# Optimization experiments

Measured on AMD Instinct MI355X. Metric: run time of the kernel, lower is better.

Reference implementation:

```python
import jax, jax.numpy as jnp
import numpy as np

N, E, H, RBF, NZ = 15000, 300000, 128, 20, 119
CUTOFF, BOX = 6.0, 7.0


def setup_inputs() -> dict:
    key = jax.random.key(0)
    ks = jax.random.split(key, 24)
    s = 0.05

    def rn(k, shape):
        return jax.random.normal(k, shape, dtype=jnp.float32) * s

    z = jax.random.randint(ks[0], (N,), 0, 83)
    pos = jax.random.uniform(ks[1], (N, 3), dtype=jnp.float32) * BOX
    src = jax.random.randint(ks[2], (E,), 0, N)
    dst = (src + jax.random.randint(ks[3], (E,), 1, N)) % N  # guarantees src != dst
    edge_index = jnp.stack([src, dst], axis=0)  # (2, E)
    cell_offsets = (jax.random.randint(ks[4], (E, 3), 0, 3) - 1).astype(jnp.float32)
    cell = jnp.eye(3, dtype=jnp.float32) * BOX
    return dict(
        z=z, pos=pos, edge_index=edge_index, cell_offsets=cell_offsets, cell=cell,
        embed=rn(ks[5], (NZ, H)),
        msg_w1=rn(ks[6], (3, H, H)), msg_b1=rn(ks[7], (3, H)),
        msg_w2=rn(ks[8], (3, H, 3 * H)), msg_b2=rn(ks[9], (3, 3 * H)),
        filt_w=rn(ks[10], (3, RBF, 3 * H)), filt_b=rn(ks[11], (3, 3 * H)),
        upd_uw=rn(ks[12], (3, H, H)), upd_ub=rn(ks[13], (3, H)),
        upd_vw=rn(ks[14], (3, H, H)), upd_vb=rn(ks[15], (3, H)),
        upd_mw1=rn(ks[16], (3, 2 * H, H)), upd_mb1=rn(ks[17], (3, H)),
        upd_mw2=rn(ks[18], (3, H, 3 * H)), upd_mb2=rn(ks[19], (3, 3 * H)),
        head_w1=rn(ks[20], (H, H)), head_b1=rn(ks[21], (H,)),
        head_w2=rn(ks[22], (H, H)), head_b2=rn(ks[23], (H,)),
    )


def reference(z, pos, edge_index, cell_offsets, cell, embed,
              msg_w1, msg_b1, msg_w2, msg_b2, filt_w, filt_b,
              upd_uw, upd_ub, upd_vw, upd_vb,
              upd_mw1, upd_mb1, upd_mw2, upd_mb2,
              head_w1, head_b1, head_w2, head_b2):
    n_nodes = z.shape[0]
    hdim = embed.shape[1]
    row, col = edge_index[0], edge_index[1]  # receiver, sender (DeepDFT convention)

    # get_pbc_distances
    offsets = cell_offsets @ cell                                  # (E,3)
    edge_diff = pos[row] - pos[col] + offsets                      # (E,3)
    edge_dist = jnp.linalg.norm(edge_diff, axis=-1)                # (E,)
    unit = edge_diff / edge_dist[:, None]                          # (E,3)

    # sinc radial basis + cosine cutoff (shared by all message layers)
    n = jnp.arange(1, RBF + 1, dtype=pos.dtype)
    rbf = jnp.sin(edge_dist[:, None] * n * jnp.pi / CUTOFF) / edge_dist[:, None]  # (E,RBF)
    fcut = jnp.where(edge_dist < CUTOFF,
                     0.5 * (jnp.cos(jnp.pi * edge_dist / CUTOFF) + 1.0), 0.0)      # (E,)

    ns = embed[z]                                                  # (N,H)
    nv = jnp.zeros((n_nodes, 3, hdim), dtype=pos.dtype)            # (N,3,H)

    for i in range(3):
        # ---- PainnMessage ----
        filt = (rbf @ filt_w[i] + filt_b[i]) * fcut[:, None]       # (E,3H)
        sout = jax.nn.silu(ns @ msg_w1[i] + msg_b1[i]) @ msg_w2[i] + msg_b2[i]  # (N,3H)
        fo = filt * sout[col]                                      # (E,3H)
        gate_v, gate_e, msg_s = jnp.split(fo, 3, axis=1)           # each (E,H)
        msg_v = nv[col] * gate_v[:, None, :] + gate_e[:, None, :] * unit[:, :, None]  # (E,3,H)
        ns = ns + jax.ops.segment_sum(msg_s, row, num_segments=n_nodes)
        nv = nv + jax.ops.segment_sum(msg_v, row, num_segments=n_nodes)
        # ---- PainnUpdate ----
        Uv = nv @ upd_uw[i] + upd_ub[i]                            # (N,3,H)
        Vv = nv @ upd_vw[i] + upd_vb[i]                            # (N,3,H)
        mlp_in = jnp.concatenate([jnp.linalg.norm(Vv, axis=1), ns], axis=1)  # (N,2H)
        m = jax.nn.silu(mlp_in @ upd_mw1[i] + upd_mb1[i]) @ upd_mw2[i] + upd_mb2[i]  # (N,3H)
        a_vv, a_sv, a_ss = jnp.split(m, 3, axis=1)
        inner = jnp.sum(Uv * Vv, axis=1)                           # (N,H)
        nv = nv + a_vv[:, None, :] * Uv
        ns = ns + a_sv * inner + a_ss

    v = jax.nn.silu(ns @ head_w1 + head_b1) @ head_w2 + head_b2    # (N,H)
    return v, edge_dist
```

## Files before the change

kernel.cpp:

```cpp
#include <hip/hip_runtime.h>
#include <math.h>

#define HD 128
#define H3 384
#define RBF_N 20
#define CUTOFF_R 6.0f
#define PI_F 3.14159265358979323846f
#define CAPE 40000

#define PITCH 136

typedef __attribute__((ext_vector_type(8))) short short8v;
typedef __attribute__((ext_vector_type(4))) short short4v;
typedef __attribute__((ext_vector_type(4))) float f32x4;
typedef unsigned short bf_t;

__device__ __forceinline__ float silu_f(float x) { return x / (1.0f + __expf(-x)); }

__device__ __forceinline__ ushort f2bf(float f) {
    union { float f; uint u; } v; v.f = f;
    return (ushort)((v.u + 0x7FFF + ((v.u >> 16) & 1)) >> 16);
}
__device__ __forceinline__ float bf2f(ushort x) {
    union { uint u; float f; } v; v.u = ((uint)x) << 16;
    return v.f;
}
__device__ __forceinline__ short4v f2bf4(float4 x) {
    short4v r;
    r[0] = (short)f2bf(x.x); r[1] = (short)f2bf(x.y);
    r[2] = (short)f2bf(x.z); r[3] = (short)f2bf(x.w);
    return r;
}
__device__ __forceinline__ float4 b2f4(short4v x) {
    return make_float4(bf2f((ushort)x[0]), bf2f((ushort)x[1]),
                       bf2f((ushort)x[2]), bf2f((ushort)x[3]));
}

#define LOADWG(r, CNT, NTH, W, rowlen, koff)                                   \
    _Pragma("unroll")                                                          \
    for (int it_ = 0; it_ < CNT; ++it_) {                                      \
        int u_ = tid + it_ * NTH;                                              \
        (r)[it_] = *(const short8v*)((W) + (size_t)(u_ >> 4) * (rowlen) +      \
                                     (koff) + ((u_ & 15) << 3));               \
    }
#define COMMITWG(r, CNT, NTH)                                                  \
    _Pragma("unroll")                                                          \
    for (int it_ = 0; it_ < CNT; ++it_) {                                      \
        int u_ = tid + it_ * NTH;                                              \
        *(short8v*)&Wt[(u_ >> 4) * PITCH + ((u_ & 15) << 3)] = (r)[it_];       \
    }
#define MFMA4R(Abuf, acc)                                                      \
    _Pragma("unroll")                                                          \
    for (int step_ = 0; step_ < 4; ++step_) {                                  \
        int kb_ = step_ * 32 + lk;                                             \
        short8v a_ = *(const short8v*)&(Abuf)[(wr + lr) * PITCH + kb_];        \
        (acc) = __builtin_amdgcn_mfma_f32_16x16x32_bf16(                       \
            a_, *(const short8v*)&Wt[(wn + lr) * PITCH + kb_], (acc), 0, 0, 0);\
    }
#define MFMA8R(Abuf, acc)                                                      \
    _Pragma("unroll")                                                          \
    for (int step_ = 0; step_ < 4; ++step_) {                                  \
        int kb_ = step_ * 32 + lk;                                             \
        short8v a_ = *(const short8v*)&(Abuf)[(wr + lr) * PITCH + kb_];        \
        (acc)[0] = __builtin_amdgcn_mfma_f32_16x16x32_bf16(                    \
            a_, *(const short8v*)&Wt[(wn + lr) * PITCH + kb_], (acc)[0], 0, 0, 0); \
        (acc)[1] = __builtin_amdgcn_mfma_f32_16x16x32_bf16(                    \
            a_, *(const short8v*)&Wt[(wn + 16 + lr) * PITCH + kb_], (acc)[1], 0, 0, 0); \
    }

__global__ void geom_kernel(const float* __restrict__ pos, const int* __restrict__ ei,
                            const float* __restrict__ cofs, const float* __restrict__ cell,
                            float* __restrict__ dist_out, int* __restrict__ deg, int E) {
    int e = blockIdx.x * blockDim.x + threadIdx.x;
    if (e >= E) return;
    int r = ei[e], c = ei[E + e];
    float c0 = cofs[3*e], c1 = cofs[3*e+1], c2 = cofs[3*e+2];
    float d0 = pos[3*r]   - pos[3*c]   + c0*cell[0] + c1*cell[3] + c2*cell[6];
    float d1 = pos[3*r+1] - pos[3*c+1] + c0*cell[1] + c1*cell[4] + c2*cell[7];
    float d2 = pos[3*r+2] - pos[3*c+2] + c0*cell[2] + c1*cell[5] + c2*cell[8];
    float dist = sqrtf(d0*d0 + d1*d1 + d2*d2);
    dist_out[e] = dist;
    if (dist < CUTOFF_R) atomicAdd(&deg[r], 1);
}

__global__ void scan_kernel(const int* __restrict__ deg, int* __restrict__ off,
                            int* __restrict__ cursor, int n) {
    __shared__ int wsum[16];
    __shared__ int carry_s;
    const int tid = threadIdx.x;
    const int lane = tid & 63, wv = tid >> 6;
    if (tid == 0) carry_s = 0;
    __syncthreads();
    for (int base = 0; base < n; base += 1024) {
        int v = (base + tid < n) ? deg[base + tid] : 0;
        int x = v;
        #pragma unroll
        for (int s = 1; s < 64; s <<= 1) {
            int y = __shfl_up(x, s);
            if (lane >= s) x += y;
        }
        if (lane == 63) wsum[wv] = x;
        __syncthreads();
        if (tid == 0) {
            int a = carry_s;
            #pragma unroll
            for (int i = 0; i < 16; ++i) { int t = wsum[i]; wsum[i] = a; a += t; }
            carry_s = a;
        }
        __syncthreads();
        int exc = wsum[wv] + x - v;
        if (base + tid < n) { off[base + tid] = exc; cursor[base + tid] = exc; }
        __syncthreads();
    }
    if (tid == 0) off[n] = carry_s;
}

__global__ void scatter_kernel(const float* __restrict__ pos, const int* __restrict__ ei,
                               const float* __restrict__ cofs, const float* __restrict__ cell,
                               const float* __restrict__ dist_in, int* __restrict__ cursor,
                               int* __restrict__ col_s, float* __restrict__ fcut_s,
                               float* __restrict__ unit_s, float* __restrict__ rbf_s, int E) {
    int e = blockIdx.x * blockDim.x + threadIdx.x;
    if (e >= E) return;
    float dist = dist_in[e];
    if (!(dist < CUTOFF_R)) return;
    int r = ei[e], c = ei[E + e];
    float c0 = cofs[3*e], c1 = cofs[3*e+1], c2 = cofs[3*e+2];
    float d0 = pos[3*r]   - pos[3*c]   + c0*cell[0] + c1*cell[3] + c2*cell[6];
    float d1 = pos[3*r+1] - pos[3*c+1] + c0*cell[1] + c1*cell[4] + c2*cell[7];
    float d2 = pos[3*r+2] - pos[3*c+2] + c0*cell[2] + c1*cell[5] + c2*cell[8];
    int p = atomicAdd(&cursor[r], 1);
    if (p >= CAPE) return;
    col_s[p] = c;
    fcut_s[p] = 0.5f * (cosf(PI_F * dist / CUTOFF_R) + 1.0f);
    float inv = 1.0f / dist;
    unit_s[3*p]   = d0 * inv;
    unit_s[3*p+1] = d1 * inv;
    unit_s[3*p+2] = d2 * inv;
    #pragma unroll
    for (int j = 0; j < RBF_N; ++j)
        rbf_s[(size_t)p*RBF_N + j] = sinf(dist * (float)(j+1) * (PI_F / CUTOFF_R)) * inv;
}

__device__ __forceinline__ void wcvt(const float* __restrict__ src, bf_t* __restrict__ dst,
                                     int idx, int K, int N) {
    int per = K * N;
    int l = idx / per, r = idx % per;
    int k = r / N, n = r % N;
    dst[(size_t)l*per + (size_t)n*K + k] = f2bf(src[(size_t)l*per + (size_t)k*N + n]);
}

__global__ void wprep_kernel(const float* s0, const float* s1, const float* s2, const float* s3,
                             const float* s4, const float* s5, const float* s6, const float* s7,
                             bf_t* __restrict__ dst) {
    int i = blockIdx.x * blockDim.x + threadIdx.x;
    if (i < 49152)        wcvt(s0, dst + 0,      i - 0,      128, 128);
    else if (i < 196608)  wcvt(s1, dst + 49152,  i - 49152,  128, 384);
    else if (i < 245760)  wcvt(s2, dst + 196608, i - 196608, 128, 128);
    else if (i < 294912)  wcvt(s3, dst + 245760, i - 245760, 128, 128);
    else if (i < 393216)  wcvt(s4, dst + 294912, i - 294912, 256, 128);
    else if (i < 540672)  wcvt(s5, dst + 393216, i - 393216, 128, 384);
    else if (i < 557056)  wcvt(s6, dst + 540672, i - 540672, 128, 128);
    else if (i < 573440)  wcvt(s7, dst + 557056, i - 557056, 128, 128);
}

__global__ __launch_bounds__(512) void msg_mlp0(const int* __restrict__ z,
                                                const float* __restrict__ emb,
                                                bf_t* __restrict__ nsb,
                                                const bf_t* __restrict__ W1b,
                                                const float* __restrict__ b1,
                                                const bf_t* __restrict__ W2b,
                                                const float* __restrict__ b2,
                                                bf_t* __restrict__ Cb, int M) {
    __shared__ ushort As[32 * PITCH];
    __shared__ ushort Wt[128 * PITCH];
    __shared__ ushort Hid[32 * PITCH];
    const int tid = threadIdx.x;
    const int m0 = blockIdx.x * 32;
    const int wid = tid >> 6, lane = tid & 63;
    const int wr = (wid >> 2) * 16;
    const int wn = (wid & 3) * 32;
    const int lr = lane & 15, lk = (lane >> 4) << 3;
    const int er = (lane >> 4) << 2;

    short8v rwA[4], rwB[4];
    LOADWG(rwA, 4, 512, W1b, 128, 0);
    {
        int row = tid >> 4, k8 = (tid & 15) << 3;
        int m = m0 + row;
        short8v pk = (short8v)(0);
        if (m < M) {
            const float* ep = emb + (size_t)z[m] * HD + k8;
            const float4 x = *(const float4*)ep, y = *(const float4*)(ep + 4);
            pk[0]=(short)f2bf(x.x); pk[1]=(short)f2bf(x.y);
            pk[2]=(short)f2bf(x.z); pk[3]=(short)f2bf(x.w);
            pk[4]=(short)f2bf(y.x); pk[5]=(short)f2bf(y.y);
            pk[6]=(short)f2bf(y.z); pk[7]=(short)f2bf(y.w);
            *(short8v*)(nsb + (size_t)m * HD + k8) = pk;
        }
        *(short8v*)&As[row * PITCH + k8] = pk;
    }
    __syncthreads();
    COMMITWG(rwA, 4, 512); LOADWG(rwB, 4, 512, W2b, 128, 0);
    __syncthreads();
    f32x4 acc1[2];
    acc1[0] = (f32x4)(0.f); acc1[1] = (f32x4)(0.f);
    MFMA8R(As, acc1);
    __syncthreads();
    COMMITWG(rwB, 4, 512); LOADWG(rwA, 4, 512, W2b + 16384, 128, 0);
    #pragma unroll
    for (int j = 0; j < 2; ++j) {
        int col = wn + 16 * j + lr;
        float bb = b1[col];
        #pragma unroll
        for (int r = 0; r < 4; ++r)
            Hid[(wr + er + r) * PITCH + col] = f2bf(silu_f(acc1[j][r] + bb));
    }
    __syncthreads();
    {
        f32x4 a0[2]; a0[0] = (f32x4)(0.f); a0[1] = (f32x4)(0.f);
        MFMA8R(Hid, a0);
        __syncthreads();
        COMMITWG(rwA, 4, 512); LOADWG(rwB, 4, 512, W2b + 32768, 128, 0);
        #pragma unroll
        for (int j = 0; j < 2; ++j) {
            int col = wn + 16 * j + lr;
            float bb = b2[col];
            #pragma unroll
            for (int r = 0; r < 4; ++r) {
                int m = m0 + wr + er + r;
                if (m < M) Cb[(size_t)m * H3 + col] = f2bf(a0[j][r] + bb);
            }
        }
        __syncthreads();
    }
    {
        f32x4 a1[2]; a1[0] = (f32x4)(0.f); a1[1] = (f32x4)(0.f);
        MFMA8R(Hid, a1);
        __syncthreads();
        COMMITWG(rwB, 4, 512);
        #pragma unroll
        for (int j = 0; j < 2; ++j) {
            int col = wn + 16 * j + lr;
            float bb = b2[128 + col];
            #pragma unroll
            for (int r = 0; r < 4; ++r) {
                int m = m0 + wr + er + r;
                if (m < M) Cb[(size_t)m * H3 + 128 + col] = f2bf(a1[j][r] + bb);
            }
        }
        __syncthreads();
    }
    {
        f32x4 a2[2]; a2[0] = (f32x4)(0.f); a2[1] = (f32x4)(0.f);
        MFMA8R(Hid, a2);
        #pragma unroll
        for (int j = 0; j < 2; ++j) {
            int col = wn + 16 * j + lr;
            float bb = b2[256 + col];
            #pragma unroll
            for (int r = 0; r < 4; ++r) {
                int m = m0 + wr + er + r;
                if (m < M) Cb[(size_t)m * H3 + 256 + col] = f2bf(a2[j][r] + bb);
            }
        }
    }
}

template <int MODE>
__global__ __launch_bounds__(1024) void upd_fused(const bf_t* __restrict__ nv2p,
                                                 const bf_t* __restrict__ Ub,
                                                 const bf_t* __restrict__ Vb,
                                                 const float* __restrict__ bu,
                                                 const float* __restrict__ bv,
                                                 bf_t* __restrict__ nvp,
                                                 bf_t* __restrict__ nsb,
                                                 const bf_t* __restrict__ W1b,
                                                 const float* __restrict__ b1,
                                                 const bf_t* __restrict__ W2b,
                                                 const float* __restrict__ b2,
                                                 const bf_t* __restrict__ xw1,
                                                 const float* __restrict__ xb1,
                                                 const bf_t* __restrict__ xw2,
                                                 const float* __restrict__ xb2,
                                                 bf_t* __restrict__ soutb,
                                                 float* __restrict__ Cf,
                                                 int N) {
    __shared__ ushort As3[3][32 * PITCH];
    __shared__ ushort Wt[128 * PITCH];
    __shared__ ushort nrmL[32 * PITCH];
    __shared__ ushort Hid[32 * PITCH];
    __shared__ ushort AsG[32 * PITCH];
    const int tid = threadIdx.x;
    const int m0 = blockIdx.x * 32;
    const int wid = tid >> 6, lane = tid & 63;
    const int wr = (wid >> 3) * 16;
    const int wn = (wid & 7) * 16;
    const int lr = lane & 15, lk = (lane >> 4) << 3;
    const int er = (lane >> 4) << 2;
    const size_t NHD = (size_t)N * HD;

    short8v rwA[2], rwB[2];
    LOADWG(rwA, 2, 1024, Ub, 128, 0);

    #pragma unroll
    for (int it = 0; it < 2; ++it) {
        int u = tid + it * 1024;
        if (u < 1536) {
            int d = u >> 9, v = u & 511;
            int row = v >> 4, k8 = (v & 15) << 3;
            int m = m0 + row;
            short8v pk = (short8v)(0);
            if (m < N) pk = *(const short8v*)(nv2p + (size_t)d * NHD + (size_t)m * HD + k8);
            *(short8v*)&As3[d][row * PITCH + k8] = pk;
        }
    }
    if (tid < 512) {
        int row = tid >> 4, k8 = (tid & 15) << 3;
        int m = m0 + row;
        short8v pk = (short8v)(0);
        if (m < N) pk = *(const short8v*)(nsb + (size_t)m * HD + k8);
        *(short8v*)&AsG[row * PITCH + k8] = pk;
    }
    __syncthreads();
    COMMITWG(rwA, 2, 1024); LOADWG(rwB, 2, 1024, Vb, 128, 0);
    __syncthreads();

    f32x4 aU[3], aV[3];
    #pragma unroll
    for (int d = 0; d < 3; ++d) { aU[d] = (f32x4)(0.f); aV[d] = (f32x4)(0.f); }
    #pragma unroll
    for (int d = 0; d < 3; ++d) { MFMA4R(As3[d], aU[d]); }
    __syncthreads();
    COMMITWG(rwB, 2, 1024); LOADWG(rwA, 2, 1024, W1b, 256, 0);
    __syncthreads();

    #pragma unroll
    for (int d = 0; d < 3; ++d) { MFMA4R(As3[d], aV[d]); }
    float inn_r[4];
    {
        int col = wn + lr;
        float bbu = bu[col], bbv = bv[col];
        #pragma unroll
        for (int r = 0; r < 4; ++r) {
            float inn = 0.f, nrm = 0.f;
            #pragma unroll
            for (int d = 0; d < 3; ++d) {
                float u = aU[d][r] + bbu;
                float v = aV[d][r] + bbv;
                aU[d][r] = u;
                inn += u * v;
                nrm += v * v;
            }
            inn_r[r] = inn;
            nrmL[(wr + er + r) * PITCH + col] = f2bf(sqrtf(nrm));
        }
    }
    __syncthreads();
    COMMITWG(rwA, 2, 1024); LOADWG(rwB, 2, 1024, W1b, 256, 128);
    __syncthreads();

    f32x4 acc1 = (f32x4)(0.f);
    MFMA4R(nrmL, acc1);
    __syncthreads();
    COMMITWG(rwB, 2, 1024);
    if (MODE == 1) { LOADWG(rwA, 2, 1024, W2b, 128, 0); }
    else           { LOADWG(rwA, 2, 1024, W2b + 16384, 128, 0); }
    __syncthreads();

    MFMA4R(AsG, acc1);
    {
        int col = wn + lr;
        float bb = b1[col];
        #pragma unroll
        for (int r = 0; r < 4; ++r)
            Hid[(wr + er + r) * PITCH + col] = f2bf(silu_f(acc1[r] + bb));
    }
    __syncthreads();
    COMMITWG(rwA, 2, 1024);
    if (MODE == 1) { LOADWG(rwB, 2, 1024, W2b + 16384, 128, 0); }
    else           { LOADWG(rwB, 2, 1024, W2b + 32768, 128, 0); }
    __syncthreads();

    float sv[4];
    if (MODE == 1) {
        f32x4 g0 = (f32x4)(0.f);
        MFMA4R(Hid, g0);
        {
            int col = wn + lr;
            float bb = b2[col];
            #pragma unroll
            for (int r = 0; r < 4; ++r) {
                int m = m0 + wr + er + r;
                if (m < N) {
                    float g = g0[r] + bb;
                    #pragma unroll
                    for (int d = 0; d < 3; ++d) {
                        float pp = bf2f(As3[d][(wr + er + r) * PITCH + col]);
                        nvp[(size_t)d * NHD + (size_t)m * HD + col] =
                            f2bf(pp + g * aU[d][r]);
                    }
                }
            }
        }
        __syncthreads();
        COMMITWG(rwB, 2, 1024); LOADWG(rwA, 2, 1024, W2b + 32768, 128, 0);
        __syncthreads();
        f32x4 g1 = (f32x4)(0.f);
        MFMA4R(Hid, g1);
        {
            int col = wn + lr;
            float bb = b2[128 + col];
            #pragma unroll
            for (int r = 0; r < 4; ++r)
                sv[r] = (g1[r] + bb) * inn_r[r];
        }
        __syncthreads();
        COMMITWG(rwA, 2, 1024); LOADWG(rwB, 2, 1024, xw1, 128, 0);
        __syncthreads();
        f32x4 g2 = (f32x4)(0.f);
        MFMA4R(Hid, g2);
        {
            int col = wn + lr;
            float bb = b2[256 + col];
            #pragma unroll
            for (int r = 0; r < 4; ++r) {
                int m = m0 + wr + er + r;
                if (m < N) {
                    int idx = (wr + er + r) * PITCH + col;
                    float s = bf2f(AsG[idx]) + sv[r] + (g2[r] + bb);
                    ushort sb = f2bf(s);
                    AsG[idx] = sb;
                    nsb[(size_t)m * HD + col] = sb;
                }
            }
        }
        __syncthreads();
        COMMITWG(rwB, 2, 1024); LOADWG(rwA, 2, 1024, xw2, 128, 0);
        __syncthreads();
        f32x4 ah = (f32x4)(0.f);
        MFMA4R(AsG, ah);
        {
            int col = wn + lr;
            float bb = xb1[col];
            #pragma unroll
            for (int r = 0; r < 4; ++r)
                Hid[(wr + er + r) * PITCH + col] = f2bf(silu_f(ah[r] + bb));
        }
        __syncthreads();
        COMMITWG(rwA, 2, 1024); LOADWG(rwB, 2, 1024, xw2 + 16384, 128, 0);
        __syncthreads();
        {
            f32x4 o0 = (f32x4)(0.f);
            MFMA4R(Hid, o0);
            int col = wn + lr;
            float bb = xb2[col];
            #pragma unroll
            for (int r = 0; r < 4; ++r) {
                int m = m0 + wr + er + r;
                if (m < N) soutb[(size_t)m * H3 + col] = f2bf(o0[r] + bb);
            }
        }
        __syncthreads();
        COMMITWG(rwB, 2, 1024); LOADWG(rwA, 2, 1024, xw2 + 32768, 128, 0);
        __syncthreads();
        {
            f32x4 o1 = (f32x4)(0.f);
            MFMA4R(Hid, o1);
            int col = wn + lr;
            float bb = xb2[128 + col];
            #pragma unroll
            for (int r = 0; r < 4; ++r) {
                int m = m0 + wr + er + r;
                if (m < N) soutb[(size_t)m * H3 + 128 + col] = f2bf(o1[r] + bb);
            }
        }
        __syncthreads();
        COMMITWG(rwA, 2, 1024);
        __syncthreads();
        {
            f32x4 o2 = (f32x4)(0.f);
            MFMA4R(Hid, o2);
            int col = wn + lr;
            float bb = xb2[256 + col];
            #pragma unroll
            for (int r = 0; r < 4; ++r) {
                int m = m0 + wr + er + r;
                if (m < N) soutb[(size_t)m * H3 + 256 + col] = f2bf(o2[r] + bb);
            }
        }
    } else {
        f32x4 g1 = (f32x4)(0.f);
        MFMA4R(Hid, g1);
        {
            int col = wn + lr;
            float bb = b2[128 + col];
            #pragma unroll
            for (int r = 0; r < 4; ++r)
                sv[r] = (g1[r] + bb) * inn_r[r];
        }
        __syncthreads();
        COMMITWG(rwB, 2, 1024); LOADWG(rwA, 2, 1024, xw1, 128, 0);
        __syncthreads();
        f32x4 g2 = (f32x4)(0.f);
        MFMA4R(Hid, g2);
        {
            int col = wn + lr;
            float bb = b2[256 + col];
            #pragma unroll
            for (int r = 0; r < 4; ++r) {
                int idx = (wr + er + r) * PITCH + col;
                float s = bf2f(AsG[idx]) + sv[r] + (g2[r] + bb);
                AsG[idx] = f2bf(s);
            }
        }
        __syncthreads();
        COMMITWG(rwA, 2, 1024); LOADWG(rwB, 2, 1024, xw2, 128, 0);
        __syncthreads();
        f32x4 ah = (f32x4)(0.f);
        MFMA4R(AsG, ah);
        {
            int col = wn + lr;
            float bb = xb1[col];
            #pragma unroll
            for (int r = 0; r < 4; ++r)
                Hid[(wr + er + r) * PITCH + col] = f2bf(silu_f(ah[r] + bb));
        }
        __syncthreads();
        COMMITWG(rwB, 2, 1024);
        __syncthreads();
        f32x4 ao = (f32x4)(0.f);
        MFMA4R(Hid, ao);
        {
            int col = wn + lr;
            float bb = xb2[col];
            #pragma unroll
            for (int r = 0; r < 4; ++r) {
                int m = m0 + wr + er + r;
                if (m < N) Cf[(size_t)m * HD + col] = ao[r] + bb;
            }
        }
    }
}

template <int FIRST>
__global__ __launch_bounds__(128) void message_kernel(
        bf_t* __restrict__ ns_b,
        const bf_t* __restrict__ nv_b, bf_t* __restrict__ nv2_b,
        const bf_t* __restrict__ sout,
        const int* __restrict__ col_s, const float* __restrict__ unit_s,
        const float* __restrict__ rbf_s, const float* __restrict__ fcut_s,
        const float* __restrict__ Wf_g, const float* __restrict__ bf_g,
        const int* __restrict__ off, int n_nodes) {
    const int t = threadIdx.x;
    const int nA = blockIdx.x * 2;
    if (nA >= n_nodes) return;
    const int nB = nA + 1;
    const bool hasB = (nB < n_nodes);
    const size_t NHD = (size_t)n_nodes * HD;

    float w0[RBF_N], w1[RBF_N], w2[RBF_N];
    #pragma unroll
    for (int r = 0; r < RBF_N; ++r) {
        w0[r] = Wf_g[r * H3 + t];
        w1[r] = Wf_g[r * H3 + HD + t];
        w2[r] = Wf_g[r * H3 + 2*HD + t];
    }
    const float bb0 = bf_g[t], bb1 = bf_g[HD + t], bb2 = bf_g[2*HD + t];

    int e0   = off[nA];
    int endA = off[nA + 1];
    int end  = hasB ? off[nB + 1] : endA;
    if (endA > CAPE) endA = CAPE;
    if (end  > CAPE) end  = CAPE;

    float aS = 0.f, a0 = 0.f, a1 = 0.f, a2 = 0.f;
    float bS = 0.f, b0 = 0.f, b1 = 0.f, b2 = 0.f;

    int e = e0;
    for (; e + 1 < end; e += 2) {
        int cX = col_s[e], cY = col_s[e + 1];
        float fcX = fcut_s[e], fcY = fcut_s[e + 1];
        float uX0 = unit_s[3*e],   uX1 = unit_s[3*e+1], uX2 = unit_s[3*e+2];
        float uY0 = unit_s[3*e+3], uY1 = unit_s[3*e+4], uY2 = unit_s[3*e+5];
        float fX0 = bb0, fX1 = bb1, fX2 = bb2;
        float fY0 = bb0, fY1 = bb1, fY2 = bb2;
        const float* rbX = rbf_s + (size_t)e * RBF_N;
        const float* rbY = rbX + RBF_N;
        #pragma unroll
        for (int r = 0; r < RBF_N; ++r) {
            float rx = rbX[r], ry = rbY[r];
            fX0 += rx * w0[r]; fY0 += ry * w0[r];
            fX1 += rx * w1[r]; fY1 += ry * w1[r];
            fX2 += rx * w2[r]; fY2 += ry * w2[r];
        }
        const bf_t* spX = sout + (size_t)cX * H3;
        const bf_t* spY = sout + (size_t)cY * H3;
        float gvX = fX0 * fcX * bf2f(spX[t]);
        float geX = fX1 * fcX * bf2f(spX[HD+t]);
        float msX = fX2 * fcX * bf2f(spX[2*HD+t]);
        float gvY = fY0 * fcY * bf2f(spY[t]);
        float geY = fY1 * fcY * bf2f(spY[HD+t]);
        float msY = fY2 * fcY * bf2f(spY[2*HD+t]);
        float vX0, vX1, vX2, vY0, vY1, vY2;
        if (FIRST) {
            vX0 = geX * uX0; vX1 = geX * uX1; vX2 = geX * uX2;
            vY0 = geY * uY0; vY1 = geY * uY1; vY2 = geY * uY2;
        } else {
            const bf_t* nvX = nv_b + (size_t)cX * HD + t;
            const bf_t* nvY = nv_b + (size_t)cY * HD + t;
            vX0 = bf2f(nvX[0])     * gvX + geX * uX0;
            vX1 = bf2f(nvX[NHD])   * gvX + geX * uX1;
            vX2 = bf2f(nvX[2*NHD]) * gvX + geX * uX2;
            vY0 = bf2f(nvY[0])     * gvY + geY * uY0;
            vY1 = bf2f(nvY[NHD])   * gvY + geY * uY1;
            vY2 = bf2f(nvY[2*NHD]) * gvY + geY * uY2;
        }
        if (e < endA) { a0 += vX0; a1 += vX1; a2 += vX2; aS += msX; }
        else          { b0 += vX0; b1 += vX1; b2 += vX2; bS += msX; }
        if (e + 1 < endA) { a0 += vY0; a1 += vY1; a2 += vY2; aS += msY; }
        else              { b0 += vY0; b1 += vY1; b2 += vY2; bS += msY; }
    }
    if (e < end) {
        int c = col_s[e];
        float fc = fcut_s[e];
        float u0 = unit_s[3*e], u1 = unit_s[3*e+1], u2 = unit_s[3*e+2];
        float f0 = bb0, f1 = bb1, f2 = bb2;
        const float* rb = rbf_s + (size_t)e * RBF_N;
        #pragma unroll
        for (int r = 0; r < RBF_N; ++r) {
            float rv = rb[r];
            f0 += rv * w0[r];
            f1 += rv * w1[r];
            f2 += rv * w2[r];
        }
        const bf_t* sp = sout + (size_t)c * H3;
        float gv = f0 * fc * bf2f(sp[t]);
        float ge = f1 * fc * bf2f(sp[HD+t]);
        float ms = f2 * fc * bf2f(sp[2*HD+t]);
        float v0, v1, v2;
        if (FIRST) {
            v0 = ge * u0; v1 = ge * u1; v2 = ge * u2;
        } else {
            const bf_t* nvc = nv_b + (size_t)c * HD + t;
            v0 = bf2f(nvc[0])     * gv + ge * u0;
            v1 = bf2f(nvc[NHD])   * gv + ge * u1;
            v2 = bf2f(nvc[2*NHD]) * gv + ge * u2;
        }
        if (e < endA) { a0 += v0; a1 += v1; a2 += v2; aS += ms; }
        else          { b0 += v0; b1 += v1; b2 += v2; bS += ms; }
    }

    {
        size_t b = (size_t)nA * HD + t;
        if (FIRST) {
            nv2_b[b]         = f2bf(a0);
            nv2_b[b + NHD]   = f2bf(a1);
            nv2_b[b + 2*NHD] = f2bf(a2);
        } else {
            nv2_b[b]         = f2bf(bf2f(nv_b[b])         + a0);
            nv2_b[b + NHD]   = f2bf(bf2f(nv_b[b + NHD])   + a1);
            nv2_b[b + 2*NHD] = f2bf(bf2f(nv_b[b + 2*NHD]) + a2);
        }
        if (endA > e0) {
            size_t so = (size_t)nA * HD + t;
            ns_b[so] = f2bf(bf2f(ns_b[so]) + aS);
        }
    }
    if (hasB) {
        size_t b = (size_t)nB * HD + t;
        if (FIRST) {
            nv2_b[b]         = f2bf(b0);
            nv2_b[b + NHD]   = f2bf(b1);
            nv2_b[b + 2*NHD] = f2bf(b2);
        } else {
            nv2_b[b]         = f2bf(bf2f(nv_b[b])         + b0);
            nv2_b[b + NHD]   = f2bf(bf2f(nv_b[b + NHD])   + b1);
            nv2_b[b + 2*NHD] = f2bf(bf2f(nv_b[b + 2*NHD]) + b2);
        }
        if (end > endA) {
            size_t so = (size_t)nB * HD + t;
            ns_b[so] = f2bf(bf2f(ns_b[so]) + bS);
        }
    }
}

extern "C" void kernel_launch(void* const* d_in, const int* in_sizes, int n_in,
                              void* d_out, int out_size, void* d_ws, size_t ws_size,
                              hipStream_t stream) {
    const int*   z       = (const int*)  d_in[0];
    const float* pos     = (const float*)d_in[1];
    const int*   ei      = (const int*)  d_in[2];
    const float* cofs    = (const float*)d_in[3];
    const float* cell    = (const float*)d_in[4];
    const float* emb     = (const float*)d_in[5];
    const float* msg_w1  = (const float*)d_in[6];
    const float* msg_b1  = (const float*)d_in[7];
    const float* msg_w2  = (const float*)d_in[8];
    const float* msg_b2  = (const float*)d_in[9];
    const float* filt_w  = (const float*)d_in[10];
    const float* filt_b  = (const float*)d_in[11];
    const float* upd_uw  = (const float*)d_in[12];
    const float* upd_ub  = (const float*)d_in[13];
    const float* upd_vw  = (const float*)d_in[14];
    const float* upd_vb  = (const float*)d_in[15];
    const float* upd_mw1 = (const float*)d_in[16];
    const float* upd_mb1 = (const float*)d_in[17];
    const float* upd_mw2 = (const float*)d_in[18];
    const float* upd_mb2 = (const float*)d_in[19];
    const float* head_w1 = (const float*)d_in[20];
    const float* head_b1 = (const float*)d_in[21];
    const float* head_w2 = (const float*)d_in[22];
    const float* head_b2 = (const float*)d_in[23];

    const int N = in_sizes[0];
    const int E = in_sizes[2] / 2;

    float* out_v    = (float*)d_out;
    float* out_dist = out_v + (size_t)N * HD;

    char* p = (char*)d_ws;
    auto alloc = [&](size_t bytes) -> void* {
        void* r = (void*)p;
        p += (bytes + 255) & ~(size_t)255;
        return r;
    };
    bf_t*  ns_b   = (bf_t*) alloc((size_t)N * HD * 2);
    bf_t*  nv_b   = (bf_t*) alloc((size_t)N * H3 * 2);
    bf_t*  nv2_b  = (bf_t*) alloc((size_t)N * H3 * 2);
    bf_t*  sout   = (bf_t*) alloc((size_t)N * H3 * 2);
    bf_t*  wb     = (bf_t*) alloc((size_t)573440 * 2);
    float* rbf_s  = (float*)alloc((size_t)CAPE * RBF_N * 4);
    float* fcut_s = (float*)alloc((size_t)CAPE * 4);
    float* unit_s = (float*)alloc((size_t)CAPE * 3 * 4);
    int*   col_s  = (int*)  alloc((size_t)CAPE * 4);
    int*   deg    = (int*)  alloc((size_t)N * 4);
    int*   off    = (int*)  alloc((size_t)(N + 1) * 4);
    int*   cursor = (int*)  alloc((size_t)N * 4);

    hipMemsetAsync(deg, 0, (size_t)N * 4, stream);

    int eb = (E + 255) / 256;
    geom_kernel<<<eb, 256, 0, stream>>>(pos, ei, cofs, cell, out_dist, deg, E);
    scan_kernel<<<1, 1024, 0, stream>>>(deg, off, cursor, N);
    scatter_kernel<<<eb, 256, 0, stream>>>(pos, ei, cofs, cell, out_dist, cursor,
                                           col_s, fcut_s, unit_s, rbf_s, E);
    wprep_kernel<<<(573440 + 255) / 256, 256, 0, stream>>>(
        msg_w1, msg_w2, upd_uw, upd_vw, upd_mw1, upd_mw2, head_w1, head_w2, wb);

    const bf_t* w_msg1 = wb + 0;
    const bf_t* w_msg2 = wb + 49152;
    const bf_t* w_uw   = wb + 196608;
    const bf_t* w_vw   = wb + 245760;
    const bf_t* w_mw1  = wb + 294912;
    const bf_t* w_mw2  = wb + 393216;
    const bf_t* w_hw1  = wb + 540672;
    const bf_t* w_hw2  = wb + 557056;

    int mt32 = (N + 31) / 32;
    int mpairs = (N + 1) / 2;

    msg_mlp0<<<mt32, 512, 0, stream>>>(
        z, emb, ns_b, w_msg1, msg_b1, w_msg2, msg_b2, sout, N);

    for (int i = 0; i < 3; ++i) {
        if (i == 0)
            message_kernel<1><<<mpairs, 128, 0, stream>>>(
                ns_b, nv_b, nv2_b, sout, col_s, unit_s, rbf_s, fcut_s,
                filt_w + (size_t)i*RBF_N*H3, filt_b + (size_t)i*H3, off, N);
        else
            message_kernel<0><<<mpairs, 128, 0, stream>>>(
                ns_b, nv_b, nv2_b, sout, col_s, unit_s, rbf_s, fcut_s,
                filt_w + (size_t)i*RBF_N*H3, filt_b + (size_t)i*H3, off, N);
        if (i < 2) {
            upd_fused<1><<<mt32, 1024, 0, stream>>>(
                nv2_b, w_uw + (size_t)i*16384, w_vw + (size_t)i*16384,
                upd_ub + (size_t)i*HD, upd_vb + (size_t)i*HD,
                nv_b, ns_b,
                w_mw1 + (size_t)i*32768, upd_mb1 + (size_t)i*HD,
                w_mw2 + (size_t)i*49152, upd_mb2 + (size_t)i*H3,
                w_msg1 + (size_t)(i+1)*16384, msg_b1 + (size_t)(i+1)*HD,
                w_msg2 + (size_t)(i+1)*49152, msg_b2 + (size_t)(i+1)*H3,
                sout, nullptr, N);
        } else {
            upd_fused<3><<<mt32, 1024, 0, stream>>>(
                nv2_b, w_uw + (size_t)i*16384, w_vw + (size_t)i*16384,
                upd_ub + (size_t)i*HD, upd_vb + (size_t)i*HD,
                nv_b, ns_b,
                w_mw1 + (size_t)i*32768, upd_mb1 + (size_t)i*HD,
                w_mw2 + (size_t)i*49152, upd_mb2 + (size_t)i*H3,
                w_hw1, head_b1, w_hw2, head_b2,
                nullptr, out_v, N);
        }
    }
}
```

Baseline: 225.5 us.

## Double-buffer weight tiles in upd_fused and store filter weights as bf16

```diff
diff --git a/kernel.cpp b/kernel.cpp
--- a/kernel.cpp
+++ b/kernel.cpp
@@ -43,19 +43,19 @@
         (r)[it_] = *(const short8v*)((W) + (size_t)(u_ >> 4) * (rowlen) +      \
                                      (koff) + ((u_ & 15) << 3));               \
     }
-#define COMMITWG(r, CNT, NTH)                                                  \
+#define COMMITB(r, CNT, NTH, WT)                                               \
     _Pragma("unroll")                                                          \
     for (int it_ = 0; it_ < CNT; ++it_) {                                      \
         int u_ = tid + it_ * NTH;                                              \
-        *(short8v*)&Wt[(u_ >> 4) * PITCH + ((u_ & 15) << 3)] = (r)[it_];       \
-    }
-#define MFMA4R(Abuf, acc)                                                      \
+        *(short8v*)&WT[(u_ >> 4) * PITCH + ((u_ & 15) << 3)] = (r)[it_];       \
+    }
+#define MFMA4B(Abuf, acc, WT)                                                  \
     _Pragma("unroll")                                                          \
     for (int step_ = 0; step_ < 4; ++step_) {                                  \
         int kb_ = step_ * 32 + lk;                                             \
         short8v a_ = *(const short8v*)&(Abuf)[(wr + lr) * PITCH + kb_];        \
         (acc) = __builtin_amdgcn_mfma_f32_16x16x32_bf16(                       \
-            a_, *(const short8v*)&Wt[(wn + lr) * PITCH + kb_], (acc), 0, 0, 0);\
+            a_, *(const short8v*)&WT[(wn + lr) * PITCH + kb_], (acc), 0, 0, 0);\
     }
 #define MFMA8R(Abuf, acc)                                                      \
     _Pragma("unroll")                                                          \
@@ -66,6 +66,12 @@
             a_, *(const short8v*)&Wt[(wn + lr) * PITCH + kb_], (acc)[0], 0, 0, 0); \
         (acc)[1] = __builtin_amdgcn_mfma_f32_16x16x32_bf16(                    \
             a_, *(const short8v*)&Wt[(wn + 16 + lr) * PITCH + kb_], (acc)[1], 0, 0, 0); \
+    }
+#define COMMITWG(r, CNT, NTH)                                                  \
+    _Pragma("unroll")                                                          \
+    for (int it_ = 0; it_ < CNT; ++it_) {                                      \
+        int u_ = tid + it_ * NTH;                                              \
+        *(short8v*)&Wt[(u_ >> 4) * PITCH + ((u_ & 15) << 3)] = (r)[it_];       \
     }
 
 __global__ void geom_kernel(const float* __restrict__ pos, const int* __restrict__ ei,
@@ -152,6 +158,7 @@
 
 __global__ void wprep_kernel(const float* s0, const float* s1, const float* s2, const float* s3,
                              const float* s4, const float* s5, const float* s6, const float* s7,
+                             const float* s8,
                              bf_t* __restrict__ dst) {
     int i = blockIdx.x * blockDim.x + threadIdx.x;
     if (i < 49152)        wcvt(s0, dst + 0,      i - 0,      128, 128);
@@ -162,6 +169,7 @@
     else if (i < 540672)  wcvt(s5, dst + 393216, i - 393216, 128, 384);
     else if (i < 557056)  wcvt(s6, dst + 540672, i - 540672, 128, 128);
     else if (i < 573440)  wcvt(s7, dst + 557056, i - 557056, 128, 128);
+    else if (i < 596480)  dst[i] = f2bf(s8[i - 573440]);
 }
 
 __global__ __launch_bounds__(512) void msg_mlp0(const int* __restrict__ z,
@@ -287,7 +295,8 @@
                                                  float* __restrict__ Cf,
                                                  int N) {
     __shared__ ushort As3[3][32 * PITCH];
-    __shared__ ushort Wt[128 * PITCH];
+    __shared__ ushort Wt0[128 * PITCH];
+    __shared__ ushort Wt1[128 * PITCH];
     __shared__ ushort nrmL[32 * PITCH];
     __shared__ ushort Hid[32 * PITCH];
     __shared__ ushort AsG[32 * PITCH];
@@ -323,20 +332,19 @@
         *(short8v*)&AsG[row * PITCH + k8] = pk;
     }
     __syncthreads();
-    COMMITWG(rwA, 2, 1024); LOADWG(rwB, 2, 1024, Vb, 128, 0);
+    COMMITB(rwA, 2, 1024, Wt0); LOADWG(rwB, 2, 1024, Vb, 128, 0);
     __syncthreads();
 
     f32x4 aU[3], aV[3];
     #pragma unroll
     for (int d = 0; d < 3; ++d) { aU[d] = (f32x4)(0.f); aV[d] = (f32x4)(0.f); }
     #pragma unroll
-    for (int d = 0; d < 3; ++d) { MFMA4R(As3[d], aU[d]); }
-    __syncthreads();
-    COMMITWG(rwB, 2, 1024); LOADWG(rwA, 2, 1024, W1b, 256, 0);
+    for (int d = 0; d < 3; ++d) { MFMA4B(As3[d], aU[d], Wt0); }
+    COMMITB(rwB, 2, 1024, Wt1); LOADWG(rwA, 2, 1024, W1b, 256, 0);
     __syncthreads();
 
     #pragma unroll
-    for (int d = 0; d < 3; ++d) { MFMA4R(As3[d], aV[d]); }
+    for (int d = 0; d < 3; ++d) { MFMA4B(As3[d], aV[d], Wt1); }
     float inn_r[4];
     {
         int col = wn + lr;
@@ -356,19 +364,17 @@
             nrmL[(wr + er + r) * PITCH + col] = f2bf(sqrtf(nrm));
         }
     }
-    __syncthreads();
-    COMMITWG(rwA, 2, 1024); LOADWG(rwB, 2, 1024, W1b, 256, 128);
+    COMMITB(rwA, 2, 1024, Wt0); LOADWG(rwB, 2, 1024, W1b, 256, 128);
     __syncthreads();
 
     f32x4 acc1 = (f32x4)(0.f);
-    MFMA4R(nrmL, acc1);
-    __syncthreads();
-    COMMITWG(rwB, 2, 1024);
+    MFMA4B(nrmL, acc1, Wt0);
+    COMMITB(rwB, 2, 1024, Wt1);
     if (MODE == 1) { LOADWG(rwA, 2, 1024, W2b, 128, 0); }
     else           { LOADWG(rwA, 2, 1024, W2b + 16384, 128, 0); }
     __syncthreads();
 
-    MFMA4R(AsG, acc1);
+    MFMA4B(AsG, acc1, Wt1);
     {
         int col = wn + lr;
         float bb = b1[col];
@@ -376,8 +382,7 @@
         for (int r = 0; r < 4; ++r)
             Hid[(wr + er + r) * PITCH + col] = f2bf(silu_f(acc1[r] + bb));
     }
-    __syncthreads();
-    COMMITWG(rwA, 2, 1024);
+    COMMITB(rwA, 2, 1024, Wt0);
     if (MODE == 1) { LOADWG(rwB, 2, 1024, W2b + 16384, 128, 0); }
     else           { LOADWG(rwB, 2, 1024, W2b + 32768, 128, 0); }
     __syncthreads();
@@ -385,7 +390,7 @@
     float sv[4];
     if (MODE == 1) {
         f32x4 g0 = (f32x4)(0.f);
-        MFMA4R(Hid, g0);
+        MFMA4B(Hid, g0, Wt0);
         {
             int col = wn + lr;
             float bb = b2[col];
@@ -403,11 +408,10 @@
                 }
             }
         }
-        __syncthreads();
-        COMMITWG(rwB, 2, 1024); LOADWG(rwA, 2, 1024, W2b + 32768, 128, 0);
+        COMMITB(rwB, 2, 1024, Wt1); LOADWG(rwA, 2, 1024, W2b + 32768, 128, 0);
         __syncthreads();
         f32x4 g1 = (f32x4)(0.f);
-        MFMA4R(Hid, g1);
+        MFMA4B(Hid, g1, Wt1);
         {
             int col = wn + lr;
             float bb = b2[128 + col];
@@ -415,11 +419,10 @@
             for (int r = 0; r < 4; ++r)
                 sv[r] = (g1[r] + bb) * inn_r[r];
         }
-        __syncthreads();
-        COMMITWG(rwA, 2, 1024); LOADWG(rwB, 2, 1024, xw1, 128, 0);
+        COMMITB(rwA, 2, 1024, Wt0); LOADWG(rwB, 2, 1024, xw1, 128, 0);
         __syncthreads();
         f32x4 g2 = (f32x4)(0.f);
-        MFMA4R(Hid, g2);
+        MFMA4B(Hid, g2, Wt0);
         {
             int col = wn + lr;
             float bb = b2[256 + col];
@@ -435,11 +438,10 @@
                 }
             }
         }
-        __syncthreads();
-        COMMITWG(rwB, 2, 1024); LOADWG(rwA, 2, 1024, xw2, 128, 0);
+        COMMITB(rwB, 2, 1024, Wt1); LOADWG(rwA, 2, 1024, xw2, 128, 0);
         __syncthreads();
         f32x4 ah = (f32x4)(0.f);
-        MFMA4R(AsG, ah);
+        MFMA4B(AsG, ah, Wt1);
         {
             int col = wn + lr;
             float bb = xb1[col];
@@ -447,12 +449,11 @@
             for (int r = 0; r < 4; ++r)
                 Hid[(wr + er + r) * PITCH + col] = f2bf(silu_f(ah[r] + bb));
         }
-        __syncthreads();
-        COMMITWG(rwA, 2, 1024); LOADWG(rwB, 2, 1024, xw2 + 16384, 128, 0);
+        COMMITB(rwA, 2, 1024, Wt0); LOADWG(rwB, 2, 1024, xw2 + 16384, 128, 0);
         __syncthreads();
         {
             f32x4 o0 = (f32x4)(0.f);
-            MFMA4R(Hid, o0);
+            MFMA4B(Hid, o0, Wt0);
             int col = wn + lr;
             float bb = xb2[col];
             #pragma unroll
@@ -461,12 +462,11 @@
                 if (m < N) soutb[(size_t)m * H3 + col] = f2bf(o0[r] + bb);
             }
         }
-        __syncthreads();
-        COMMITWG(rwB, 2, 1024); LOADWG(rwA, 2, 1024, xw2 + 32768, 128, 0);
+        COMMITB(rwB, 2, 1024, Wt1); LOADWG(rwA, 2, 1024, xw2 + 32768, 128, 0);
         __syncthreads();
         {
             f32x4 o1 = (f32x4)(0.f);
-            MFMA4R(Hid, o1);
+            MFMA4B(Hid, o1, Wt1);
             int col = wn + lr;
             float bb = xb2[128 + col];
             #pragma unroll
@@ -475,12 +475,11 @@
                 if (m < N) soutb[(size_t)m * H3 + 128 + col] = f2bf(o1[r] + bb);
             }
         }
-        __syncthreads();
-        COMMITWG(rwA, 2, 1024);
+        COMMITB(rwA, 2, 1024, Wt0);
         __syncthreads();
         {
             f32x4 o2 = (f32x4)(0.f);
-            MFMA4R(Hid, o2);
+            MFMA4B(Hid, o2, Wt0);
             int col = wn + lr;
             float bb = xb2[256 + col];
             #pragma unroll
@@ -491,7 +490,7 @@
         }
     } else {
         f32x4 g1 = (f32x4)(0.f);
-        MFMA4R(Hid, g1);
+        MFMA4B(Hid, g1, Wt0);
         {
             int col = wn + lr;
             float bb = b2[128 + col];
@@ -499,11 +498,10 @@
             for (int r = 0; r < 4; ++r)
                 sv[r] = (g1[r] + bb) * inn_r[r];
         }
-        __syncthreads();
-        COMMITWG(rwB, 2, 1024); LOADWG(rwA, 2, 1024, xw1, 128, 0);
+        COMMITB(rwB, 2, 1024, Wt1); LOADWG(rwA, 2, 1024, xw1, 128, 0);
         __syncthreads();
         f32x4 g2 = (f32x4)(0.f);
-        MFMA4R(Hid, g2);
+        MFMA4B(Hid, g2, Wt1);
         {
             int col = wn + lr;
             float bb = b2[256 + col];
@@ -514,11 +512,10 @@
                 AsG[idx] = f2bf(s);
             }
         }
-        __syncthreads();
-        COMMITWG(rwA, 2, 1024); LOADWG(rwB, 2, 1024, xw2, 128, 0);
+        COMMITB(rwA, 2, 1024, Wt0); LOADWG(rwB, 2, 1024, xw2, 128, 0);
         __syncthreads();
         f32x4 ah = (f32x4)(0.f);
-        MFMA4R(AsG, ah);
+        MFMA4B(AsG, ah, Wt0);
         {
             int col = wn + lr;
             float bb = xb1[col];
@@ -526,11 +523,10 @@
             for (int r = 0; r < 4; ++r)
                 Hid[(wr + er + r) * PITCH + col] = f2bf(silu_f(ah[r] + bb));
         }
-        __syncthreads();
-        COMMITWG(rwB, 2, 1024);
+        COMMITB(rwB, 2, 1024, Wt1);
         __syncthreads();
         f32x4 ao = (f32x4)(0.f);
-        MFMA4R(Hid, ao);
+        MFMA4B(Hid, ao, Wt1);
         {
             int col = wn + lr;
             float bb = xb2[col];
@@ -550,7 +546,7 @@
         const bf_t* __restrict__ sout,
         const int* __restrict__ col_s, const float* __restrict__ unit_s,
         const float* __restrict__ rbf_s, const float* __restrict__ fcut_s,
-        const float* __restrict__ Wf_g, const float* __restrict__ bf_g,
+        const bf_t* __restrict__ Wf_b, const float* __restrict__ bf_g,
         const int* __restrict__ off, int n_nodes) {
     const int t = threadIdx.x;
     const int nA = blockIdx.x * 2;
@@ -562,9 +558,9 @@
     float w0[RBF_N], w1[RBF_N], w2[RBF_N];
     #pragma unroll
     for (int r = 0; r < RBF_N; ++r) {
-        w0[r] = Wf_g[r * H3 + t];
-        w1[r] = Wf_g[r * H3 + HD + t];
-        w2[r] = Wf_g[r * H3 + 2*HD + t];
+        w0[r] = bf2f(Wf_b[r * H3 + t]);
+        w1[r] = bf2f(Wf_b[r * H3 + HD + t]);
+        w2[r] = bf2f(Wf_b[r * H3 + 2*HD + t]);
     }
     const float bb0 = bf_g[t], bb1 = bf_g[HD + t], bb2 = bf_g[2*HD + t];
 
@@ -729,7 +725,7 @@
     bf_t*  nv_b   = (bf_t*) alloc((size_t)N * H3 * 2);
     bf_t*  nv2_b  = (bf_t*) alloc((size_t)N * H3 * 2);
     bf_t*  sout   = (bf_t*) alloc((size_t)N * H3 * 2);
-    bf_t*  wb     = (bf_t*) alloc((size_t)573440 * 2);
+    bf_t*  wb     = (bf_t*) alloc((size_t)596480 * 2);
     float* rbf_s  = (float*)alloc((size_t)CAPE * RBF_N * 4);
     float* fcut_s = (float*)alloc((size_t)CAPE * 4);
     float* unit_s = (float*)alloc((size_t)CAPE * 3 * 4);
@@ -745,8 +741,8 @@
     scan_kernel<<<1, 1024, 0, stream>>>(deg, off, cursor, N);
     scatter_kernel<<<eb, 256, 0, stream>>>(pos, ei, cofs, cell, out_dist, cursor,
                                            col_s, fcut_s, unit_s, rbf_s, E);
-    wprep_kernel<<<(573440 + 255) / 256, 256, 0, stream>>>(
-        msg_w1, msg_w2, upd_uw, upd_vw, upd_mw1, upd_mw2, head_w1, head_w2, wb);
+    wprep_kernel<<<(596480 + 255) / 256, 256, 0, stream>>>(
+        msg_w1, msg_w2, upd_uw, upd_vw, upd_mw1, upd_mw2, head_w1, head_w2, filt_w, wb);
 
     const bf_t* w_msg1 = wb + 0;
     const bf_t* w_msg2 = wb + 49152;
@@ -756,6 +752,7 @@
     const bf_t* w_mw2  = wb + 393216;
     const bf_t* w_hw1  = wb + 540672;
     const bf_t* w_hw2  = wb + 557056;
+    const bf_t* w_fw   = wb + 573440;
 
     int mt32 = (N + 31) / 32;
     int mpairs = (N + 1) / 2;
@@ -767,11 +764,11 @@
         if (i == 0)
             message_kernel<1><<<mpairs, 128, 0, stream>>>(
                 ns_b, nv_b, nv2_b, sout, col_s, unit_s, rbf_s, fcut_s,
-                filt_w + (size_t)i*RBF_N*H3, filt_b + (size_t)i*H3, off, N);
+                w_fw + (size_t)i*RBF_N*H3, filt_b + (size_t)i*H3, off, N);
         else
             message_kernel<0><<<mpairs, 128, 0, stream>>>(
                 ns_b, nv_b, nv2_b, sout, col_s, unit_s, rbf_s, fcut_s,
-                filt_w + (size_t)i*RBF_N*H3, filt_b + (size_t)i*H3, off, N);
+                w_fw + (size_t)i*RBF_N*H3, filt_b + (size_t)i*H3, off, N);
         if (i < 2) {
             upd_fused<1><<<mt32, 1024, 0, stream>>>(
                 nv2_b, w_uw + (size_t)i*16384, w_vw + (size_t)i*16384,
```

New measurement: 217.5 us. 1.04x faster.
